# Kernel optimization log

Measured on AMD Instinct MI355X. Metric: run time of the kernel, lower is better.

## Reference

```python
import jax, jax.numpy as jnp
import numpy as np

N, E, G = 50000, 800000, 64
IN, HID, HEADS, OUT = 128, 64, 4, 128
NEG = 0.2  # PyG GATConv default negative_slope


def setup_inputs() -> dict:
    key = jax.random.key(0)
    ks = jax.random.split(key, 12)
    nrm = lambda k, shape, s: (jax.random.normal(k, shape, jnp.float32) * s)
    x = nrm(ks[0], (N, IN), 1.0)
    edge_index = jax.random.randint(ks[1], (2, E), 0, N)
    batch = jnp.sort(jax.random.randint(ks[2], (N,), 0, G))
    W1 = nrm(ks[3], (IN, HEADS * HID), IN ** -0.5)
    a1_src = nrm(ks[4], (HEADS, HID), HID ** -0.5)
    a1_dst = nrm(ks[5], (HEADS, HID), HID ** -0.5)
    b1 = jnp.zeros((HEADS * HID,), jnp.float32)
    W2 = nrm(ks[6], (HEADS * HID, OUT), (HEADS * HID) ** -0.5)
    a2_src = nrm(ks[7], (1, OUT), OUT ** -0.5)
    a2_dst = nrm(ks[8], (1, OUT), OUT ** -0.5)
    b2 = jnp.zeros((OUT,), jnp.float32)
    fc_W = nrm(ks[9], (OUT, OUT), OUT ** -0.5)
    fc_b = jnp.zeros((OUT,), jnp.float32)
    return dict(x=x, edge_index=edge_index, batch=batch, W1=W1, a1_src=a1_src,
                a1_dst=a1_dst, b1=b1, W2=W2, a2_src=a2_src, a2_dst=a2_dst,
                b2=b2, fc_W=fc_W, fc_b=fc_b)


def gat_conv(x, W, a_src, a_dst, b, src, dst, heads):
    n = x.shape[0]
    ch = W.shape[1] // heads
    h = (x @ W).reshape(n, heads, ch)                      # [n, H, C]
    al_s = jnp.einsum('nhc,hc->nh', h, a_src)              # per-node src logits
    al_d = jnp.einsum('nhc,hc->nh', h, a_dst)
    e = al_s[src] + al_d[dst]                              # [E, H]
    e = jnp.where(e > 0, e, NEG * e)                       # LeakyReLU
    # segment softmax over incoming edges of each dst node
    m = jax.lax.stop_gradient(jax.ops.segment_max(e, dst, num_segments=n))
    m = jnp.where(jnp.isfinite(m), m, 0.0)
    ex = jnp.exp(e - m[dst])
    s = jax.ops.segment_sum(ex, dst, num_segments=n)
    alpha = ex / (s[dst] + 1e-16)                          # [E, H]
    out = jax.ops.segment_sum(h[src] * alpha[..., None], dst, num_segments=n)
    return out.reshape(n, heads * ch) + b                  # concat heads + bias


def reference(x, edge_index, batch, W1, a1_src, a1_dst, b1, W2, a2_src, a2_dst, b2, fc_W, fc_b):
    loops = jnp.arange(N, dtype=edge_index.dtype)          # PyG adds self-loops
    src = jnp.concatenate([edge_index[0], loops])
    dst = jnp.concatenate([edge_index[1], loops])
    h = jax.nn.elu(gat_conv(x, W1, a1_src, a1_dst, b1, src, dst, HEADS))
    h = jax.nn.elu(gat_conv(h, W2, a2_src, a2_dst, b2, src, dst, 1))
    sums = jax.ops.segment_sum(h, batch, num_segments=G)
    cnt = jax.ops.segment_sum(jnp.ones((N,), h.dtype), batch, num_segments=G)
    pooled = sums / jnp.maximum(cnt, 1.0)[:, None]         # global mean pool
    return jax.nn.relu(pooled @ fc_W + fc_b)
```

## Files before the change

kernel.cpp:

```cpp
#include <hip/hip_runtime.h>
#include <math.h>

#define N_NODES 50000
#define N_EDGES 800000
#define N_GRAPHS 64
#define NEG 0.2f

typedef unsigned short us;
typedef us us2 __attribute__((ext_vector_type(2)));
typedef us us4 __attribute__((ext_vector_type(4)));
typedef us us8 __attribute__((ext_vector_type(8)));
typedef short bf16x8 __attribute__((ext_vector_type(8)));
typedef float f32x4 __attribute__((ext_vector_type(4)));

__device__ __forceinline__ us bf16rn(float f) {
  unsigned int u = __float_as_uint(f);
  u += 0x7FFFu + ((u >> 16) & 1u);
  return (us)(u >> 16);
}
__device__ __forceinline__ float bf2f(us h) {
  return __uint_as_float(((unsigned int)h) << 16);
}
__device__ __forceinline__ float readlane_f(float v, int l) {
  return __uint_as_float((unsigned)__builtin_amdgcn_readlane(__float_as_uint(v), l));
}

__global__ __launch_bounds__(256) void xsplit_kernel(const float* __restrict__ x,
                                                     us* __restrict__ xh,
                                                     us* __restrict__ xl,
                                                     int total4) {
  int i = blockIdx.x * 256 + threadIdx.x;
  if (i >= total4) return;
  float4 v = *(const float4*)&x[(size_t)i * 4];
  us h0 = bf16rn(v.x), h1 = bf16rn(v.y), h2 = bf16rn(v.z), h3 = bf16rn(v.w);
  us4 hv = {h0, h1, h2, h3};
  us4 lv = {bf16rn(v.x - bf2f(h0)), bf16rn(v.y - bf2f(h1)),
            bf16rn(v.z - bf2f(h2)), bf16rn(v.w - bf2f(h3))};
  *(us4*)&xh[(size_t)i * 4] = hv;
  *(us4*)&xl[(size_t)i * 4] = lv;
}

__global__ __launch_bounds__(256) void convW_kernel(
    const float* __restrict__ W1, const float* __restrict__ W2,
    us* __restrict__ w1h, us* __restrict__ w1l,
    us* __restrict__ w2h, us* __restrict__ w2l) {
  int idx = blockIdx.x * 256 + threadIdx.x;
  const float* W; us *oh, *ol; int K, N, li;
  if (idx < 128 * 256) {
    W = W1; oh = w1h; ol = w1l; K = 128; N = 256; li = idx;
  } else if (idx < 2 * 128 * 256) {
    W = W2; oh = w2h; ol = w2l; K = 256; N = 128; li = idx - 128 * 256;
  } else return;
  int n = li / K, k = li - n * K;
  float f = W[(size_t)k * N + n];
  us h = bf16rn(f);
  oh[li] = h;
  ol[li] = bf16rn(f - bf2f(h));
}

__global__ __launch_bounds__(256, 2) void gemm_bf16x3(
    const us* __restrict__ Agh, const us* __restrict__ Agl,
    const us* __restrict__ Bth, const us* __restrict__ Btl,
    us* __restrict__ C, int M, int N, int K) {
  __shared__ us Ah[128][40];
  __shared__ us Al[128][40];
  __shared__ us Bh[128][40];
  __shared__ us Bl[128][40];
  int t = threadIdx.x;
  int m0 = blockIdx.x * 128;
  int n0 = blockIdx.y * 128;
  int w = t >> 6, l = t & 63;
  int wr = w >> 1, wc = w & 1;
  int l15 = l & 15, g = l >> 4;

  f32x4 acc[4][4] = {};

  for (int kb = 0; kb < K; kb += 32) {
    us8 z = {};
    #pragma unroll
    for (int i = 0; i < 2; i++) {
      int slot = i * 256 + t;
      int row = slot >> 2, kq = slot & 3;
      size_t gi = (size_t)(m0 + row) * K + kb + kq * 8;
      bool ok = (m0 + row) < M;
      *(us8*)&Ah[row][kq * 8] = ok ? *(const us8*)&Agh[gi] : z;
      *(us8*)&Al[row][kq * 8] = ok ? *(const us8*)&Agl[gi] : z;
    }
    #pragma unroll
    for (int i = 0; i < 2; i++) {
      int slot = i * 256 + t;
      int n = slot >> 2, kq = slot & 3;
      size_t gi = (size_t)(n0 + n) * K + kb + kq * 8;
      *(us8*)&Bh[n][kq * 8] = *(const us8*)&Bth[gi];
      *(us8*)&Bl[n][kq * 8] = *(const us8*)&Btl[gi];
    }
    __syncthreads();

    bf16x8 af[4], al4[4], bf[4], bl4[4];
    #pragma unroll
    for (int i = 0; i < 4; i++) {
      af[i]  = *(const bf16x8*)&Ah[wr * 64 + i * 16 + l15][g * 8];
      al4[i] = *(const bf16x8*)&Al[wr * 64 + i * 16 + l15][g * 8];
      bf[i]  = *(const bf16x8*)&Bh[wc * 64 + i * 16 + l15][g * 8];
      bl4[i] = *(const bf16x8*)&Bl[wc * 64 + i * 16 + l15][g * 8];
    }
    #pragma unroll
    for (int i = 0; i < 4; i++)
      #pragma unroll
      for (int j = 0; j < 4; j++) {
        acc[i][j] = __builtin_amdgcn_mfma_f32_16x16x32_bf16(af[i], bf[j], acc[i][j], 0, 0, 0);
        acc[i][j] = __builtin_amdgcn_mfma_f32_16x16x32_bf16(af[i], bl4[j], acc[i][j], 0, 0, 0);
        acc[i][j] = __builtin_amdgcn_mfma_f32_16x16x32_bf16(al4[i], bf[j], acc[i][j], 0, 0, 0);
      }
    __syncthreads();
  }

  #pragma unroll
  for (int i = 0; i < 4; i++)
    #pragma unroll
    for (int j = 0; j < 4; j++)
      #pragma unroll
      for (int r = 0; r < 4; r++) {
        int row = m0 + wr * 64 + i * 16 + g * 4 + r;
        if (row < M) {
          int col = n0 + wc * 64 + j * 16 + l15;
          C[(size_t)row * N + col] = bf16rn(acc[i][j][r]);
        }
      }
}

__global__ __launch_bounds__(256) void logits1_kernel(
    const us* __restrict__ h1b, const float* __restrict__ a_src,
    const float* __restrict__ a_dst, float* __restrict__ al_s,
    float* __restrict__ al_d) {
  int idx = blockIdx.x * 256 + threadIdx.x;
  if (idx >= N_NODES * 4) return;
  int n = idx >> 2, h = idx & 3;
  const us* hp = &h1b[(size_t)n * 256 + h * 64];
  float ss = 0.f, sd = 0.f;
  #pragma unroll
  for (int i = 0; i < 8; i++) {
    us8 v = *(const us8*)&hp[i * 8];
    #pragma unroll
    for (int j = 0; j < 8; j++) {
      float f = bf2f(v[j]);
      ss += f * a_src[h * 64 + i * 8 + j];
      sd += f * a_dst[h * 64 + i * 8 + j];
    }
  }
  al_s[idx] = ss;
  al_d[idx] = sd;
}

__global__ __launch_bounds__(256) void logits2_kernel(
    const us* __restrict__ h2b, const float* __restrict__ a_src,
    const float* __restrict__ a_dst, float* __restrict__ al_s,
    float* __restrict__ al_d) {
  int n = blockIdx.x * 256 + threadIdx.x;
  if (n >= N_NODES) return;
  const us* hp = &h2b[(size_t)n * 128];
  float ss = 0.f, sd = 0.f;
  #pragma unroll
  for (int i = 0; i < 16; i++) {
    us8 v = *(const us8*)&hp[i * 8];
    #pragma unroll
    for (int j = 0; j < 8; j++) {
      float f = bf2f(v[j]);
      ss += f * a_src[i * 8 + j];
      sd += f * a_dst[i * 8 + j];
    }
  }
  al_s[n] = ss;
  al_d[n] = sd;
}

__global__ __launch_bounds__(256) void count_kernel(const int* __restrict__ dst,
                                                    int* __restrict__ cnt) {
  int e = blockIdx.x * 256 + threadIdx.x;
  if (e < N_EDGES) atomicAdd(&cnt[dst[e]], 1);
}

__global__ __launch_bounds__(256) void scan1_kernel(const int* __restrict__ cnt,
                                                    int* __restrict__ itmp,
                                                    int* __restrict__ bsum) {
  int i = blockIdx.x * 256 + threadIdx.x;
  int v = (i < N_NODES) ? cnt[i] : 0;
  int lane = threadIdx.x & 63, w = threadIdx.x >> 6;
  int s = v;
  #pragma unroll
  for (int off = 1; off < 64; off <<= 1) {
    int tv = __shfl_up(s, off);
    if (lane >= off) s += tv;
  }
  __shared__ int wsum[4];
  if (lane == 63) wsum[w] = s;
  __syncthreads();
  int add = 0;
  for (int p = 0; p < w; p++) add += wsum[p];
  s += add;
  if (i < N_NODES) itmp[i] = s;
  if (threadIdx.x == 255) bsum[blockIdx.x] = s;
}

__global__ __launch_bounds__(256) void scan2_kernel(const int* __restrict__ bsum,
                                                    int* __restrict__ boff,
                                                    int nb) {
  int t = threadIdx.x;
  int v = (t < nb) ? bsum[t] : 0;
  int lane = t & 63, w = t >> 6;
  int s = v;
  #pragma unroll
  for (int off = 1; off < 64; off <<= 1) {
    int tv = __shfl_up(s, off);
    if (lane >= off) s += tv;
  }
  __shared__ int wsum[4];
  if (lane == 63) wsum[w] = s;
  __syncthreads();
  int add = 0;
  for (int p = 0; p < w; p++) add += wsum[p];
  s += add;
  if (t < nb) boff[t] = s - v;
}

__global__ __launch_bounds__(256) void scan3_kernel(const int* __restrict__ cnt,
                                                    const int* __restrict__ itmp,
                                                    const int* __restrict__ boff,
                                                    int* __restrict__ rowst,
                                                    int* __restrict__ cursor) {
  int i = blockIdx.x * 256 + threadIdx.x;
  if (i < N_NODES) {
    int excl = itmp[i] - cnt[i] + boff[i >> 8];
    rowst[i] = excl;
    cursor[i] = excl;
  }
  if (i == 0) rowst[N_NODES] = N_EDGES;
}

__global__ __launch_bounds__(256) void scatter_kernel(
    const int* __restrict__ src, const int* __restrict__ dst,
    int* __restrict__ cursor, int* __restrict__ csr_src) {
  int e = blockIdx.x * 256 + threadIdx.x;
  if (e < N_EDGES) {
    int p = atomicAdd(&cursor[dst[e]], 1);
    csr_src[p] = src[e];
  }
}

__global__ __launch_bounds__(256) void agg1_kernel(
    const us* __restrict__ h1b, const float* __restrict__ al_s,
    const float* __restrict__ al_d, const int* __restrict__ rowst,
    const int* __restrict__ csrc, const float* __restrict__ b1,
    us* __restrict__ outh, us* __restrict__ outl) {
  int d = (blockIdx.x * 256 + threadIdx.x) >> 6;
  int lane = threadIdx.x & 63;
  if (d >= N_NODES) return;
  int head = lane >> 4;
  int c0 = lane * 4;
  int wsel = lane & 48;
  float ald = al_d[d * 4 + head];
  float wsum = 0.f, a0 = 0.f, a1 = 0.f, a2 = 0.f, a3 = 0.f;
  {
    float v = al_s[d * 4 + head] + ald;
    v = v > 0.f ? v : NEG * v;
    float w = __expf(v);
    us4 hv = *(const us4*)&h1b[(size_t)d * 256 + c0];
    wsum += w;
    a0 += w * bf2f(hv[0]); a1 += w * bf2f(hv[1]);
    a2 += w * bf2f(hv[2]); a3 += w * bf2f(hv[3]);
  }
  int beg = rowst[d], end = rowst[d + 1];
  int j = beg;
  for (; j + 16 <= end; j += 16) {
    int el = lane & 15;
    int sv = csrc[j + el];
    float v = al_s[sv * 4 + head] + ald;
    v = v > 0.f ? v : NEG * v;
    float wv = __expf(v);
    #pragma unroll
    for (int half = 0; half < 2; ++half) {
      int ss[8]; us4 hv[8];
      #pragma unroll
      for (int k = 0; k < 8; ++k)
        ss[k] = __builtin_amdgcn_readlane(sv, half * 8 + k);
      #pragma unroll
      for (int k = 0; k < 8; ++k)
        hv[k] = *(const us4*)&h1b[(size_t)(unsigned)ss[k] * 256 + c0];
      #pragma unroll
      for (int k = 0; k < 8; ++k) {
        float w = __shfl(wv, half * 8 + k + wsel);
        wsum += w;
        a0 += w * bf2f(hv[k][0]); a1 += w * bf2f(hv[k][1]);
        a2 += w * bf2f(hv[k][2]); a3 += w * bf2f(hv[k][3]);
      }
    }
  }
  int m = end - j;
  if (m > 0) {
    int el = lane & 15;
    int sv = csrc[j + (el < m ? el : 0)];
    float v = al_s[sv * 4 + head] + ald;
    v = v > 0.f ? v : NEG * v;
    float wv = __expf(v);
    for (int b = 0; b < m; b += 8) {
      int ss[8]; us4 hv[8];
      #pragma unroll
      for (int k = 0; k < 8; ++k) {
        int kk = b + k;
        ss[k] = __builtin_amdgcn_readlane(sv, kk < m ? kk : 0);
      }
      #pragma unroll
      for (int k = 0; k < 8; ++k)
        hv[k] = *(const us4*)&h1b[(size_t)(unsigned)ss[k] * 256 + c0];
      #pragma unroll
      for (int k = 0; k < 8; ++k) {
        int kk = b + k;
        float w = __shfl(wv, (kk < m ? kk : 0) + wsel);
        if (kk >= m) w = 0.f;
        wsum += w;
        a0 += w * bf2f(hv[k][0]); a1 += w * bf2f(hv[k][1]);
        a2 += w * bf2f(hv[k][2]); a3 += w * bf2f(hv[k][3]);
      }
    }
  }
  float inv = 1.f / (wsum + 1e-16f);
  float4 bb = *(const float4*)&b1[c0];
  float o[4] = {a0 * inv + bb.x, a1 * inv + bb.y, a2 * inv + bb.z, a3 * inv + bb.w};
  us4 oh, ol;
  #pragma unroll
  for (int i = 0; i < 4; i++) {
    float e = o[i] > 0.f ? o[i] : expm1f(o[i]);
    us h = bf16rn(e);
    oh[i] = h;
    ol[i] = bf16rn(e - bf2f(h));
  }
  *(us4*)&outh[(size_t)d * 256 + c0] = oh;
  *(us4*)&outl[(size_t)d * 256 + c0] = ol;
}

__global__ __launch_bounds__(256) void agg2_kernel(
    const us* __restrict__ h2b, const float* __restrict__ al_s,
    const float* __restrict__ al_d, const int* __restrict__ rowst,
    const int* __restrict__ csrc, const float* __restrict__ b2,
    float* __restrict__ out) {
  int d = (blockIdx.x * 256 + threadIdx.x) >> 6;
  int lane = threadIdx.x & 63;
  if (d >= N_NODES) return;
  int c0 = lane * 2;
  float ald = al_d[d];
  float wsum = 0.f, a0 = 0.f, a1 = 0.f;
  {
    float v = al_s[d] + ald;
    v = v > 0.f ? v : NEG * v;
    float w = __expf(v);
    us2 hv = *(const us2*)&h2b[(size_t)d * 128 + c0];
    wsum += w;
    a0 += w * bf2f(hv[0]); a1 += w * bf2f(hv[1]);
  }
  int beg = rowst[d], end = rowst[d + 1];
  for (int j = beg; j < end; j += 64) {
    int m = end - j;
    m = m < 64 ? m : 64;
    int sv = csrc[j + (lane < m ? lane : 0)];
    float v = al_s[sv] + ald;
    v = v > 0.f ? v : NEG * v;
    float wv = __expf(v);
    for (int b = 0; b < m; b += 8) {
      int ss[8]; us2 hv[8];
      #pragma unroll
      for (int k = 0; k < 8; ++k) {
        int kk = b + k;
        ss[k] = __builtin_amdgcn_readlane(sv, kk < m ? kk : 0);
      }
      #pragma unroll
      for (int k = 0; k < 8; ++k)
        hv[k] = *(const us2*)&h2b[(size_t)(unsigned)ss[k] * 128 + c0];
      #pragma unroll
      for (int k = 0; k < 8; ++k) {
        int kk = b + k;
        float w = readlane_f(wv, kk < m ? kk : 0);
        if (kk >= m) w = 0.f;
        wsum += w;
        a0 += w * bf2f(hv[k][0]); a1 += w * bf2f(hv[k][1]);
      }
    }
  }
  float inv = 1.f / (wsum + 1e-16f);
  float2 bb = *(const float2*)&b2[c0];
  float o0 = a0 * inv + bb.x, o1 = a1 * inv + bb.y;
  o0 = o0 > 0.f ? o0 : expm1f(o0);
  o1 = o1 > 0.f ? o1 : expm1f(o1);
  *(float2*)&out[(size_t)d * 128 + c0] = make_float2(o0, o1);
}

#define PNPB 128
__global__ __launch_bounds__(256) void pool_kernel(const float* __restrict__ y,
                                                   const int* __restrict__ batch,
                                                   float* __restrict__ psum) {
  int t = threadIdx.x;
  int lane32 = t & 31;
  int sub = t >> 5;
  int base = blockIdx.x * PNPB + sub * (PNPB / 8);
  int nend = base + PNPB / 8;
  if (nend > N_NODES) nend = N_NODES;
  float4 acc = make_float4(0.f, 0.f, 0.f, 0.f);
  int curg = -1;
  for (int n = base; n < nend; ++n) {
    int g = batch[n];
    if (g != curg) {
      if (curg >= 0) {
        float* p = &psum[curg * 128 + lane32 * 4];
        atomicAdd(p + 0, acc.x); atomicAdd(p + 1, acc.y);
        atomicAdd(p + 2, acc.z); atomicAdd(p + 3, acc.w);
      }
      acc = make_float4(0.f, 0.f, 0.f, 0.f);
      curg = g;
    }
    float4 v = *(const float4*)&y[(size_t)n * 128 + lane32 * 4];
    acc.x += v.x; acc.y += v.y; acc.z += v.z; acc.w += v.w;
  }
  if (curg >= 0) {
    float* p = &psum[curg * 128 + lane32 * 4];
    atomicAdd(p + 0, acc.x); atomicAdd(p + 1, acc.y);
    atomicAdd(p + 2, acc.z); atomicAdd(p + 3, acc.w);
  }
}

__global__ __launch_bounds__(128) void fc_kernel(
    const float* __restrict__ psum, const int* __restrict__ batch,
    const float* __restrict__ fcW, const float* __restrict__ fcb,
    float* __restrict__ out) {
  __shared__ float pr[128];
  __shared__ int bounds[2];
  int g = blockIdx.x, c = threadIdx.x;
  if (c < 2) {
    int target = g + c;
    int lo = 0, hi = N_NODES;
    while (lo < hi) {
      int mid = (lo + hi) >> 1;
      if (batch[mid] < target) lo = mid + 1; else hi = mid;
    }
    bounds[c] = lo;
  }
  __syncthreads();
  float cnt = (float)(bounds[1] - bounds[0]);
  cnt = cnt > 1.f ? cnt : 1.f;
  pr[c] = psum[g * 128 + c] / cnt;
  __syncthreads();
  float s = fcb[c];
  #pragma unroll 8
  for (int k = 0; k < 128; k++) s += pr[k] * fcW[k * 128 + c];
  out[g * 128 + c] = fmaxf(s, 0.f);
}

extern "C" void kernel_launch(void* const* d_in, const int* in_sizes, int n_in,
                              void* d_out, int out_size, void* d_ws,
                              size_t ws_size, hipStream_t stream) {
  const float* x      = (const float*)d_in[0];
  const int*   ei     = (const int*)d_in[1];
  const int*   batch  = (const int*)d_in[2];
  const float* W1     = (const float*)d_in[3];
  const float* a1_src = (const float*)d_in[4];
  const float* a1_dst = (const float*)d_in[5];
  const float* b1     = (const float*)d_in[6];
  const float* W2     = (const float*)d_in[7];
  const float* a2_src = (const float*)d_in[8];
  const float* a2_dst = (const float*)d_in[9];
  const float* b2     = (const float*)d_in[10];
  const float* fc_W   = (const float*)d_in[11];
  const float* fc_b   = (const float*)d_in[12];
  float* out = (float*)d_out;

  const int* srcp = ei;
  const int* dstp = ei + N_EDGES;
  const int NB = (N_NODES + 255) / 256;

  float* y    = (float*)d_ws;
  float* al1s = y + (size_t)N_NODES * 128;
  float* al1d = al1s + N_NODES * 4;
  float* al2s = al1d + N_NODES * 4;
  float* al2d = al2s + N_NODES;
  float* psum = al2d + N_NODES;
  us* xh   = (us*)(psum + N_GRAPHS * 128);
  us* xl   = xh + (size_t)N_NODES * 128;
  us* x2h  = xl + (size_t)N_NODES * 128;
  us* x2l  = x2h + (size_t)N_NODES * 256;
  us* h1b  = x2l + (size_t)N_NODES * 256;
  us* h2b  = h1b + (size_t)N_NODES * 256;
  us* w1th = h2b + (size_t)N_NODES * 128;
  us* w1tl = w1th + 256 * 128;
  us* w2th = w1tl + 256 * 128;
  us* w2tl = w2th + 128 * 256;
  int* cnt    = (int*)(w2tl + 128 * 256);
  int* bsum   = cnt + N_NODES;
  int* boff   = bsum + 256;
  int* itmp   = boff + 256;
  int* rowst  = itmp + N_NODES;
  int* cursor = rowst + N_NODES + 8;
  int* csrc   = cursor + N_NODES;
  size_t needed = (size_t)((char*)(csrc + N_EDGES) - (char*)d_ws);
  if (ws_size < needed) return;

  hipMemsetAsync(cnt, 0, N_NODES * sizeof(int), stream);
  hipMemsetAsync(psum, 0, N_GRAPHS * 128 * sizeof(float), stream);

  count_kernel<<<(N_EDGES + 255) / 256, 256, 0, stream>>>(dstp, cnt);
  scan1_kernel<<<NB, 256, 0, stream>>>(cnt, itmp, bsum);
  scan2_kernel<<<1, 256, 0, stream>>>(bsum, boff, NB);
  scan3_kernel<<<NB, 256, 0, stream>>>(cnt, itmp, boff, rowst, cursor);
  scatter_kernel<<<(N_EDGES + 255) / 256, 256, 0, stream>>>(srcp, dstp, cursor, csrc);

  xsplit_kernel<<<(N_NODES * 128 / 4 + 255) / 256, 256, 0, stream>>>(
      x, xh, xl, N_NODES * 128 / 4);
  convW_kernel<<<(2 * 128 * 256 + 255) / 256, 256, 0, stream>>>(
      W1, W2, w1th, w1tl, w2th, w2tl);

  gemm_bf16x3<<<dim3(391, 2), 256, 0, stream>>>(xh, xl, w1th, w1tl, h1b, N_NODES, 256, 128);
  logits1_kernel<<<(N_NODES * 4 + 255) / 256, 256, 0, stream>>>(h1b, a1_src, a1_dst, al1s, al1d);
  agg1_kernel<<<(N_NODES * 64 + 255) / 256, 256, 0, stream>>>(
      h1b, al1s, al1d, rowst, csrc, b1, x2h, x2l);

  gemm_bf16x3<<<dim3(391, 1), 256, 0, stream>>>(x2h, x2l, w2th, w2tl, h2b, N_NODES, 128, 256);
  logits2_kernel<<<(N_NODES + 255) / 256, 256, 0, stream>>>(h2b, a2_src, a2_dst, al2s, al2d);
  agg2_kernel<<<(N_NODES * 64 + 255) / 256, 256, 0, stream>>>(
      h2b, al2s, al2d, rowst, csrc, b2, y);

  pool_kernel<<<(N_NODES + PNPB - 1) / PNPB, 256, 0, stream>>>(y, batch, psum);
  fc_kernel<<<N_GRAPHS, 128, 0, stream>>>(psum, batch, fc_W, fc_b, out);
}
```

Measured before the change: 327.4 us.

## Stage GEMM output through LDS, regroup aggregation loops, replace memsets with init kernel

The GEMM epilogue now writes bf16 results into shared memory and then stores full 16-byte rows, instead of scattered 2-byte stores per accumulator element. Both aggregation kernels restructure their gather loops into groups of four neighbours with tree-summed partial products. Layer 2 also gains a full-64 fast path without per-element bounds masking. The two hipMemsetAsync calls become one init kernel, removing a launch. Risks include an extra LDS round-trip and barrier in the GEMM, and reduced memory-level parallelism in aggregation, since fewer gathers are in flight per batch.

```diff
diff --git a/kernel.cpp b/kernel.cpp
--- a/kernel.cpp
+++ b/kernel.cpp
@@ -23,6 +23,13 @@
 }
 __device__ __forceinline__ float readlane_f(float v, int l) {
   return __uint_as_float((unsigned)__builtin_amdgcn_readlane(__float_as_uint(v), l));
+}
+
+__global__ __launch_bounds__(256) void init_kernel(int* __restrict__ cnt,
+                                                   float* __restrict__ psum) {
+  int i = blockIdx.x * 256 + threadIdx.x;
+  if (i < N_NODES) cnt[i] = 0;
+  if (i < N_GRAPHS * 128) psum[i] = 0.f;
 }
 
 __global__ __launch_bounds__(256) void xsplit_kernel(const float* __restrict__ x,
@@ -62,10 +69,7 @@
     const us* __restrict__ Agh, const us* __restrict__ Agl,
     const us* __restrict__ Bth, const us* __restrict__ Btl,
     us* __restrict__ C, int M, int N, int K) {
-  __shared__ us Ah[128][40];
-  __shared__ us Al[128][40];
-  __shared__ us Bh[128][40];
-  __shared__ us Bl[128][40];
+  __shared__ us smem[4][128][40];
   int t = threadIdx.x;
   int m0 = blockIdx.x * 128;
   int n0 = blockIdx.y * 128;
@@ -83,26 +87,26 @@
       int row = slot >> 2, kq = slot & 3;
       size_t gi = (size_t)(m0 + row) * K + kb + kq * 8;
       bool ok = (m0 + row) < M;
-      *(us8*)&Ah[row][kq * 8] = ok ? *(const us8*)&Agh[gi] : z;
-      *(us8*)&Al[row][kq * 8] = ok ? *(const us8*)&Agl[gi] : z;
+      *(us8*)&smem[0][row][kq * 8] = ok ? *(const us8*)&Agh[gi] : z;
+      *(us8*)&smem[1][row][kq * 8] = ok ? *(const us8*)&Agl[gi] : z;
     }
     #pragma unroll
     for (int i = 0; i < 2; i++) {
       int slot = i * 256 + t;
       int n = slot >> 2, kq = slot & 3;
       size_t gi = (size_t)(n0 + n) * K + kb + kq * 8;
-      *(us8*)&Bh[n][kq * 8] = *(const us8*)&Bth[gi];
-      *(us8*)&Bl[n][kq * 8] = *(const us8*)&Btl[gi];
+      *(us8*)&smem[2][n][kq * 8] = *(const us8*)&Bth[gi];
+      *(us8*)&smem[3][n][kq * 8] = *(const us8*)&Btl[gi];
     }
     __syncthreads();
 
     bf16x8 af[4], al4[4], bf[4], bl4[4];
     #pragma unroll
     for (int i = 0; i < 4; i++) {
-      af[i]  = *(const bf16x8*)&Ah[wr * 64 + i * 16 + l15][g * 8];
-      al4[i] = *(const bf16x8*)&Al[wr * 64 + i * 16 + l15][g * 8];
-      bf[i]  = *(const bf16x8*)&Bh[wc * 64 + i * 16 + l15][g * 8];
-      bl4[i] = *(const bf16x8*)&Bl[wc * 64 + i * 16 + l15][g * 8];
+      af[i]  = *(const bf16x8*)&smem[0][wr * 64 + i * 16 + l15][g * 8];
+      al4[i] = *(const bf16x8*)&smem[1][wr * 64 + i * 16 + l15][g * 8];
+      bf[i]  = *(const bf16x8*)&smem[2][wc * 64 + i * 16 + l15][g * 8];
+      bl4[i] = *(const bf16x8*)&smem[3][wc * 64 + i * 16 + l15][g * 8];
     }
     #pragma unroll
     for (int i = 0; i < 4; i++)
@@ -115,18 +119,27 @@
     __syncthreads();
   }
 
+  us* ct = &smem[0][0][0];
   #pragma unroll
   for (int i = 0; i < 4; i++)
     #pragma unroll
     for (int j = 0; j < 4; j++)
       #pragma unroll
       for (int r = 0; r < 4; r++) {
-        int row = m0 + wr * 64 + i * 16 + g * 4 + r;
-        if (row < M) {
-          int col = n0 + wc * 64 + j * 16 + l15;
-          C[(size_t)row * N + col] = bf16rn(acc[i][j][r]);
-        }
+        int row = wr * 64 + i * 16 + g * 4 + r;
+        int col = wc * 64 + j * 16 + l15;
+        ct[row * 128 + col] = bf16rn(acc[i][j][r]);
       }
+  __syncthreads();
+  #pragma unroll
+  for (int q = 0; q < 8; q++) {
+    int slot = q * 256 + t;
+    int row = slot >> 4, col8 = slot & 15;
+    if (m0 + row < M) {
+      us8 v = *(const us8*)&ct[row * 128 + col8 * 8];
+      *(us8*)&C[(size_t)(m0 + row) * N + n0 + col8 * 8] = v;
+    }
+  }
 }
 
 __global__ __launch_bounds__(256) void logits1_kernel(
@@ -278,21 +291,24 @@
     v = v > 0.f ? v : NEG * v;
     float wv = __expf(v);
     #pragma unroll
-    for (int half = 0; half < 2; ++half) {
-      int ss[8]; us4 hv[8];
-      #pragma unroll
-      for (int k = 0; k < 8; ++k)
-        ss[k] = __builtin_amdgcn_readlane(sv, half * 8 + k);
-      #pragma unroll
-      for (int k = 0; k < 8; ++k)
-        hv[k] = *(const us4*)&h1b[(size_t)(unsigned)ss[k] * 256 + c0];
-      #pragma unroll
-      for (int k = 0; k < 8; ++k) {
-        float w = __shfl(wv, half * 8 + k + wsel);
-        wsum += w;
-        a0 += w * bf2f(hv[k][0]); a1 += w * bf2f(hv[k][1]);
-        a2 += w * bf2f(hv[k][2]); a3 += w * bf2f(hv[k][3]);
-      }
+    for (int q = 0; q < 16; q += 4) {
+      int s0 = __builtin_amdgcn_readlane(sv, q + 0);
+      int s1 = __builtin_amdgcn_readlane(sv, q + 1);
+      int s2 = __builtin_amdgcn_readlane(sv, q + 2);
+      int s3 = __builtin_amdgcn_readlane(sv, q + 3);
+      us4 h0 = *(const us4*)&h1b[(size_t)(unsigned)s0 * 256 + c0];
+      us4 h1 = *(const us4*)&h1b[(size_t)(unsigned)s1 * 256 + c0];
+      us4 h2 = *(const us4*)&h1b[(size_t)(unsigned)s2 * 256 + c0];
+      us4 h3 = *(const us4*)&h1b[(size_t)(unsigned)s3 * 256 + c0];
+      float w0 = __shfl(wv, q + 0 + wsel);
+      float w1 = __shfl(wv, q + 1 + wsel);
+      float w2 = __shfl(wv, q + 2 + wsel);
+      float w3 = __shfl(wv, q + 3 + wsel);
+      wsum += w0 + w1 + w2 + w3;
+      a0 += w0 * bf2f(h0[0]) + w1 * bf2f(h1[0]) + w2 * bf2f(h2[0]) + w3 * bf2f(h3[0]);
+      a1 += w0 * bf2f(h0[1]) + w1 * bf2f(h1[1]) + w2 * bf2f(h2[1]) + w3 * bf2f(h3[1]);
+      a2 += w0 * bf2f(h0[2]) + w1 * bf2f(h1[2]) + w2 * bf2f(h2[2]) + w3 * bf2f(h3[2]);
+      a3 += w0 * bf2f(h0[3]) + w1 * bf2f(h1[3]) + w2 * bf2f(h2[3]) + w3 * bf2f(h3[3]);
     }
   }
   int m = end - j;
@@ -302,25 +318,29 @@
     float v = al_s[sv * 4 + head] + ald;
     v = v > 0.f ? v : NEG * v;
     float wv = __expf(v);
-    for (int b = 0; b < m; b += 8) {
-      int ss[8]; us4 hv[8];
-      #pragma unroll
-      for (int k = 0; k < 8; ++k) {
-        int kk = b + k;
-        ss[k] = __builtin_amdgcn_readlane(sv, kk < m ? kk : 0);
-      }
-      #pragma unroll
-      for (int k = 0; k < 8; ++k)
-        hv[k] = *(const us4*)&h1b[(size_t)(unsigned)ss[k] * 256 + c0];
-      #pragma unroll
-      for (int k = 0; k < 8; ++k) {
-        int kk = b + k;
-        float w = __shfl(wv, (kk < m ? kk : 0) + wsel);
-        if (kk >= m) w = 0.f;
-        wsum += w;
-        a0 += w * bf2f(hv[k][0]); a1 += w * bf2f(hv[k][1]);
-        a2 += w * bf2f(hv[k][2]); a3 += w * bf2f(hv[k][3]);
-      }
+    for (int q = 0; q < m; q += 4) {
+      int k0 = q, k1 = q + 1 < m ? q + 1 : 0, k2 = q + 2 < m ? q + 2 : 0,
+          k3 = q + 3 < m ? q + 3 : 0;
+      int s0 = __builtin_amdgcn_readlane(sv, k0);
+      int s1 = __builtin_amdgcn_readlane(sv, k1);
+      int s2 = __builtin_amdgcn_readlane(sv, k2);
+      int s3 = __builtin_amdgcn_readlane(sv, k3);
+      us4 h0 = *(const us4*)&h1b[(size_t)(unsigned)s0 * 256 + c0];
+      us4 h1 = *(const us4*)&h1b[(size_t)(unsigned)s1 * 256 + c0];
+      us4 h2 = *(const us4*)&h1b[(size_t)(unsigned)s2 * 256 + c0];
+      us4 h3 = *(const us4*)&h1b[(size_t)(unsigned)s3 * 256 + c0];
+      float w0 = __shfl(wv, k0 + wsel);
+      float w1 = __shfl(wv, k1 + wsel);
+      float w2 = __shfl(wv, k2 + wsel);
+      float w3 = __shfl(wv, k3 + wsel);
+      if (q + 1 >= m) w1 = 0.f;
+      if (q + 2 >= m) w2 = 0.f;
+      if (q + 3 >= m) w3 = 0.f;
+      wsum += w0 + w1 + w2 + w3;
+      a0 += w0 * bf2f(h0[0]) + w1 * bf2f(h1[0]) + w2 * bf2f(h2[0]) + w3 * bf2f(h3[0]);
+      a1 += w0 * bf2f(h0[1]) + w1 * bf2f(h1[1]) + w2 * bf2f(h2[1]) + w3 * bf2f(h3[1]);
+      a2 += w0 * bf2f(h0[2]) + w1 * bf2f(h1[2]) + w2 * bf2f(h2[2]) + w3 * bf2f(h3[2]);
+      a3 += w0 * bf2f(h0[3]) + w1 * bf2f(h1[3]) + w2 * bf2f(h2[3]) + w3 * bf2f(h3[3]);
     }
   }
   float inv = 1.f / (wsum + 1e-16f);
@@ -358,31 +378,57 @@
     a0 += w * bf2f(hv[0]); a1 += w * bf2f(hv[1]);
   }
   int beg = rowst[d], end = rowst[d + 1];
-  for (int j = beg; j < end; j += 64) {
-    int m = end - j;
-    m = m < 64 ? m : 64;
+  int j = beg;
+  for (; j + 64 <= end; j += 64) {
+    int sv = csrc[j + lane];
+    float v = al_s[sv] + ald;
+    v = v > 0.f ? v : NEG * v;
+    float wv = __expf(v);
+    for (int q = 0; q < 64; q += 4) {
+      int s0 = __builtin_amdgcn_readlane(sv, q + 0);
+      int s1 = __builtin_amdgcn_readlane(sv, q + 1);
+      int s2 = __builtin_amdgcn_readlane(sv, q + 2);
+      int s3 = __builtin_amdgcn_readlane(sv, q + 3);
+      us2 h0 = *(const us2*)&h2b[(size_t)(unsigned)s0 * 128 + c0];
+      us2 h1 = *(const us2*)&h2b[(size_t)(unsigned)s1 * 128 + c0];
+      us2 h2 = *(const us2*)&h2b[(size_t)(unsigned)s2 * 128 + c0];
+      us2 h3 = *(const us2*)&h2b[(size_t)(unsigned)s3 * 128 + c0];
+      float w0 = readlane_f(wv, q + 0);
+      float w1 = readlane_f(wv, q + 1);
+      float w2 = readlane_f(wv, q + 2);
+      float w3 = readlane_f(wv, q + 3);
+      wsum += w0 + w1 + w2 + w3;
+      a0 += w0 * bf2f(h0[0]) + w1 * bf2f(h1[0]) + w2 * bf2f(h2[0]) + w3 * bf2f(h3[0]);
+      a1 += w0 * bf2f(h0[1]) + w1 * bf2f(h1[1]) + w2 * bf2f(h2[1]) + w3 * bf2f(h3[1]);
+    }
+  }
+  int m = end - j;
+  if (m > 0) {
     int sv = csrc[j + (lane < m ? lane : 0)];
     float v = al_s[sv] + ald;
     v = v > 0.f ? v : NEG * v;
     float wv = __expf(v);
-    for (int b = 0; b < m; b += 8) {
-      int ss[8]; us2 hv[8];
-      #pragma unroll
-      for (int k = 0; k < 8; ++k) {
-        int kk = b + k;
-        ss[k] = __builtin_amdgcn_readlane(sv, kk < m ? kk : 0);
-      }
-      #pragma unroll
-      for (int k = 0; k < 8; ++k)
-        hv[k] = *(const us2*)&h2b[(size_t)(unsigned)ss[k] * 128 + c0];
-      #pragma unroll
-      for (int k = 0; k < 8; ++k) {
-        int kk = b + k;
-        float w = readlane_f(wv, kk < m ? kk : 0);
-        if (kk >= m) w = 0.f;
-        wsum += w;
-        a0 += w * bf2f(hv[k][0]); a1 += w * bf2f(hv[k][1]);
-      }
+    for (int q = 0; q < m; q += 4) {
+      int k0 = q, k1 = q + 1 < m ? q + 1 : 0, k2 = q + 2 < m ? q + 2 : 0,
+          k3 = q + 3 < m ? q + 3 : 0;
+      int s0 = __builtin_amdgcn_readlane(sv, k0);
+      int s1 = __builtin_amdgcn_readlane(sv, k1);
+      int s2 = __builtin_amdgcn_readlane(sv, k2);
+      int s3 = __builtin_amdgcn_readlane(sv, k3);
+      us2 h0 = *(const us2*)&h2b[(size_t)(unsigned)s0 * 128 + c0];
+      us2 h1 = *(const us2*)&h2b[(size_t)(unsigned)s1 * 128 + c0];
+      us2 h2 = *(const us2*)&h2b[(size_t)(unsigned)s2 * 128 + c0];
+      us2 h3 = *(const us2*)&h2b[(size_t)(unsigned)s3 * 128 + c0];
+      float w0 = readlane_f(wv, k0);
+      float w1 = readlane_f(wv, k1);
+      float w2 = readlane_f(wv, k2);
+      float w3 = readlane_f(wv, k3);
+      if (q + 1 >= m) w1 = 0.f;
+      if (q + 2 >= m) w2 = 0.f;
+      if (q + 3 >= m) w3 = 0.f;
+      wsum += w0 + w1 + w2 + w3;
+      a0 += w0 * bf2f(h0[0]) + w1 * bf2f(h1[0]) + w2 * bf2f(h2[0]) + w3 * bf2f(h3[0]);
+      a1 += w0 * bf2f(h0[1]) + w1 * bf2f(h1[1]) + w2 * bf2f(h2[1]) + w3 * bf2f(h3[1]);
     }
   }
   float inv = 1.f / (wsum + 1e-16f);
@@ -501,8 +547,7 @@
   size_t needed = (size_t)((char*)(csrc + N_EDGES) - (char*)d_ws);
   if (ws_size < needed) return;
 
-  hipMemsetAsync(cnt, 0, N_NODES * sizeof(int), stream);
-  hipMemsetAsync(psum, 0, N_GRAPHS * 128 * sizeof(float), stream);
+  init_kernel<<<NB, 256, 0, stream>>>(cnt, psum);
 
   count_kernel<<<(N_EDGES + 255) / 256, 256, 0, stream>>>(dstp, cnt);
   scan1_kernel<<<NB, 256, 0, stream>>>(cnt, itmp, bsum);
```

Result: faster. 313.5 us (-4.3%).
